# Optimization experiments

Measured on AMD Instinct MI355X. Metric: run time of the kernel, lower is better.

The kernel has to match this reference:

```python
import jax, jax.numpy as jnp
import numpy as np

B, N, C, H = 4, 2048, 1024, 16
D = C // H  # head_dim = 64
SCALE = D ** -0.5


def setup_inputs() -> dict:
    key = jax.random.key(0)
    ks = jax.random.split(key, 7)
    # freqs_cis = exp(i*theta): unit-modulus rotations, as in standard RoPE
    theta = jax.random.uniform(ks[1], (B, N, D // 2), jnp.float32, 0.0, 2 * np.pi)
    return {
        "x": jax.random.normal(ks[0], (B, N, C), jnp.float32),
        "freqs_cos": jnp.cos(theta),
        "freqs_sin": jnp.sin(theta),
        "attn_mask": jax.random.normal(ks[2], (1, 1, N, N), jnp.float32) * 0.1,
        "Wqkv": jax.random.normal(ks[3], (3 * C, C), jnp.float32) * (C ** -0.5),
        "Wproj": jax.random.normal(ks[4], (C, C), jnp.float32) * (C ** -0.5),
        "bproj": jnp.zeros((C,), jnp.float32),
    }


def _rope(t, cos, sin):
    # t: [B,H,N,D]; cos/sin: [B,1,N,D/2]; complex multiply on interleaved pairs
    tr = t.reshape(*t.shape[:-1], D // 2, 2)
    t0, t1 = tr[..., 0], tr[..., 1]
    out = jnp.stack([t0 * cos - t1 * sin, t0 * sin + t1 * cos], axis=-1)
    return out.reshape(t.shape)


def reference(x, freqs_cos, freqs_sin, attn_mask, Wqkv, Wproj, bproj):
    qkv = x @ Wqkv.T  # [B,N,3C]
    qkv = qkv.reshape(B, N, 3, H, D).transpose(2, 0, 3, 1, 4)  # [3,B,H,N,D]
    q, k, v = qkv[0], qkv[1], qkv[2]
    cos = freqs_cos[:, None]  # [B,1,N,D/2]
    sin = freqs_sin[:, None]
    q = _rope(q, cos, sin)
    k = _rope(k, cos, sin)
    attn = jnp.einsum("bhnd,bhmd->bhnm", q * SCALE, k) + attn_mask
    attn = jax.nn.softmax(attn, axis=-1)
    out = jnp.einsum("bhnm,bhmd->bhnd", attn, v)  # [B,H,N,D]
    out = out.transpose(0, 2, 1, 3).reshape(B, N, C)
    return out @ Wproj.T + bproj
```

## Files before the change

kernel.cpp:

```cpp
#include <hip/hip_runtime.h>
#include <hip/hip_bf16.h>
#include <stdint.h>


typedef __bf16 bf16;
typedef __bf16 bf16x4 __attribute__((ext_vector_type(4)));
typedef __bf16 bf16x8 __attribute__((ext_vector_type(8)));
typedef float  f32x4  __attribute__((ext_vector_type(4)));
typedef float  f32x16 __attribute__((ext_vector_type(16)));
typedef int    int4v  __attribute__((ext_vector_type(4)));

#define MFMA16(a, b, c) __builtin_amdgcn_mfma_f32_16x16x32_bf16((a), (b), (c), 0, 0, 0)
#define MFMA32(a, b, c) __builtin_amdgcn_mfma_f32_32x32x16_bf16((a), (b), (c), 0, 0, 0)

__device__ __forceinline__ bf16x4 cvt4s(float a, float b, float c, float d) {
  bf16x4 r;
  r[0] = (bf16)a; r[1] = (bf16)b; r[2] = (bf16)c; r[3] = (bf16)d;
  return r;
}
__device__ __forceinline__ bf16x8 cvt8(f32x4 a, f32x4 b) {
  bf16x8 r;
  r[0] = (bf16)a[0]; r[1] = (bf16)a[1]; r[2] = (bf16)a[2]; r[3] = (bf16)a[3];
  r[4] = (bf16)b[0]; r[5] = (bf16)b[1]; r[6] = (bf16)b[2]; r[7] = (bf16)b[3];
  return r;
}
__device__ __forceinline__ void gload16(const void* g, void* l) {
  __builtin_amdgcn_global_load_lds((const __attribute__((address_space(1))) void*)g,
                                   (__attribute__((address_space(3))) void*)l, 16, 0, 0);
}

__global__ __launch_bounds__(256)
void cvt_k(const float* __restrict__ W, bf16* __restrict__ Wb, float scale)
{
  const size_t i = ((size_t)blockIdx.x * 256 + threadIdx.x) * 8;
  const float* p = W + i;
  f32x4 a = *(const f32x4*)p * scale;
  f32x4 b = *(const f32x4*)(p + 4) * scale;
  *(bf16x8*)(Wb + i) = cvt8(a, b);
}

template<int MODE>
__global__ __launch_bounds__(256)
void gemm_bt(const bf16* __restrict__ A, const bf16* __restrict__ B,
             void* __restrict__ O0, bf16* __restrict__ O1, bf16* __restrict__ O2,
             const float* __restrict__ bias)
{
  constexpr int K = 1024;
  __shared__ __attribute__((aligned(16))) bf16 As[128 * 64];
  __shared__ __attribute__((aligned(16))) bf16 Bs[128 * 64];
  const int tid = threadIdx.x, lane = tid & 63, wid = tid >> 6;
  const int m0 = blockIdx.x * 128, n0 = blockIdx.y * 128;
  const int wm = (wid >> 1) * 64, wn = (wid & 1) * 64;
  const int l15 = lane & 15, lg = lane >> 4;

  f32x4 acc[4][4] = {};

  for (int k0 = 0; k0 < K; k0 += 64) {
#pragma unroll
    for (int c = 0; c < 4; ++c) {
      const int seg = wid * 4 + c;
      const int o = seg * 1024 + lane * 16;
      const int row = o >> 7, colb = o & 127;
      gload16((const char*)B + (((size_t)(n0 + row) * K + k0) << 1) + colb,
              (char*)Bs + seg * 1024);
      gload16((const char*)A + (((size_t)(m0 + row) * K + k0) << 1) + colb,
              (char*)As + seg * 1024);
    }
    __syncthreads();

    bf16x8 af[4][2], bb[4][2];
#pragma unroll
    for (int i = 0; i < 4; ++i)
#pragma unroll
      for (int kk = 0; kk < 2; ++kk) {
        af[i][kk] = *(const bf16x8*)(As + (wm + i * 16 + l15) * 64 + kk * 32 + lg * 8);
        bb[i][kk] = *(const bf16x8*)(Bs + (wn + i * 16 + l15) * 64 + kk * 32 + lg * 8);
      }
#pragma unroll
    for (int mi = 0; mi < 4; ++mi)
#pragma unroll
      for (int ni = 0; ni < 4; ++ni)
#pragma unroll
        for (int kk = 0; kk < 2; ++kk)
          acc[mi][ni] = MFMA16(af[mi][kk], bb[ni][kk], acc[mi][ni]);
    __syncthreads();
  }

#pragma unroll
  for (int mi = 0; mi < 4; ++mi)
#pragma unroll
    for (int ni = 0; ni < 4; ++ni)
#pragma unroll
      for (int r = 0; r < 4; ++r) {
        const int row = m0 + wm + mi * 16 + lg * 4 + r;
        const int col = n0 + wn + ni * 16 + l15;
        float v = acc[mi][ni][r];
        if (MODE == 0) {
          const int s = col >> 10, h = (col >> 6) & 15, d = col & 63;
          const int b = row >> 11, n = row & 2047;
          const bf16 bv = (bf16)v;
          if (s == 0)
            ((bf16*)O0)[(((size_t)(b * 16 + h) * 2048) + n) * 64 + d] = bv;
          else if (s == 1)
            O1[(((size_t)(b * 16 + h) * 2048) + n) * 64 + d] = bv;
          else
            O2[(((size_t)(b * 16 + h) * 64) + d) * 2048 + n] = bv;
        } else {
          ((float*)O0)[(size_t)row * 1024 + col] = v + bias[col];
        }
      }
}

__global__ __launch_bounds__(256)
void rope_k(bf16* __restrict__ Q, bf16* __restrict__ K,
            const float* __restrict__ C, const float* __restrict__ S)
{
  constexpr float SL = 0.125f * 1.4426950408889634f;
  const int gid = blockIdx.x * 256 + threadIdx.x;
  const int part = gid & 3;
  const int rowid = gid >> 2;
  const int n = rowid & 2047;
  const int b = rowid >> 15;
  const size_t cbase = ((size_t)(b * 2048 + n)) * 32 + part * 8;

  float cf[8], sf[8];
  *(f32x4*)cf = *(const f32x4*)(C + cbase);
  *(f32x4*)(cf + 4) = *(const f32x4*)(C + cbase + 4);
  *(f32x4*)sf = *(const f32x4*)(S + cbase);
  *(f32x4*)(sf + 4) = *(const f32x4*)(S + cbase + 4);

  bf16* qp = Q + (size_t)rowid * 64 + part * 16;
  bf16* kp = K + (size_t)rowid * 64 + part * 16;
  __attribute__((aligned(16))) bf16 buf[16];

  *(int4v*)buf = *(const int4v*)qp;
  *(int4v*)(buf + 8) = *(const int4v*)(qp + 8);
#pragma unroll
  for (int j = 0; j < 8; ++j) {
    const float t0 = (float)buf[2 * j], t1 = (float)buf[2 * j + 1];
    buf[2 * j]     = (bf16)((t0 * cf[j] - t1 * sf[j]) * SL);
    buf[2 * j + 1] = (bf16)((t0 * sf[j] + t1 * cf[j]) * SL);
  }
  *(int4v*)qp = *(int4v*)buf;
  *(int4v*)(qp + 8) = *(int4v*)(buf + 8);

  *(int4v*)buf = *(const int4v*)kp;
  *(int4v*)(buf + 8) = *(const int4v*)(kp + 8);
#pragma unroll
  for (int j = 0; j < 8; ++j) {
    const float t0 = (float)buf[2 * j], t1 = (float)buf[2 * j + 1];
    buf[2 * j]     = (bf16)(t0 * cf[j] - t1 * sf[j]);
    buf[2 * j + 1] = (bf16)(t0 * sf[j] + t1 * cf[j]);
  }
  *(int4v*)kp = *(int4v*)buf;
  *(int4v*)(kp + 8) = *(int4v*)(buf + 8);
}

template<int MM>
__global__ __launch_bounds__(256, 4)
void attn_k(const bf16* __restrict__ Q, const bf16* __restrict__ K,
            const bf16* __restrict__ VT, const void* __restrict__ Mv,
            bf16* __restrict__ O)
{
  constexpr float LOG2E = 1.4426950408889634f;
  __shared__ __attribute__((aligned(16))) bf16 SH[9216];
  bf16* Kt = SH;
  bf16* Vt = SH + 4096;

  const int tid = threadIdx.x, lane = tid & 63, w = tid >> 6;
  const int bh = blockIdx.x;
  const int q0 = blockIdx.y * 128;
  const int b = bh >> 4, h = bh & 15;
  const int l31 = lane & 31, hi = lane >> 5;
  const int swz = (l31 & 7) << 3;

  const bf16* Qb = Q + (size_t)bh * 2048 * 64;
  const bf16* Kb = K + (size_t)bh * 2048 * 64;
  const bf16* Vb = VT + (size_t)bh * 64 * 2048;
  const float* Mqf = (const float*)Mv + (size_t)(q0 + w * 32 + l31) * 2048;
  const bf16*  Mqb = (const bf16*)Mv  + (size_t)(q0 + w * 32 + l31) * 2048;

  bf16x8 qf[4];
  {
    const bf16* qr = Qb + (size_t)(q0 + w * 32 + l31) * 64 + 8 * hi;
#pragma unroll
    for (int j = 0; j < 4; ++j) qf[j] = *(const bf16x8*)(qr + 16 * j);
  }

  f32x16 o[2] = {{0,0,0,0,0,0,0,0,0,0,0,0,0,0,0,0},
                 {0,0,0,0,0,0,0,0,0,0,0,0,0,0,0,0}};
  float li = 0.f;

  for (int kv0 = 0; kv0 < 2048; kv0 += 64) {
#pragma unroll
    for (int it = 0; it < 2; ++it) {
      const int idx = it * 256 + tid;
      const int row = idx >> 3, g8 = (idx & 7) * 8;
      const int sc = g8 ^ ((row & 7) << 3);
      *(int4v*)(Kt + row * 64 + sc) =
          *(const int4v*)(Kb + (size_t)(kv0 + row) * 64 + g8);
      *(int4v*)(Vt + row * 64 + sc) =
          *(const int4v*)(Vb + (size_t)row * 2048 + kv0 + g8);
    }

    f32x4 mkf[2][4];
    bf16x4 mkb[2][4];
#pragma unroll
    for (int sub = 0; sub < 2; ++sub)
#pragma unroll
      for (int rg = 0; rg < 4; ++rg) {
        if (MM == 0)
          mkf[sub][rg] = *(const f32x4*)(Mqf + kv0 + 32 * sub + 8 * rg + 4 * hi);
        else
          mkb[sub][rg] = *(const bf16x4*)(Mqb + kv0 + 32 * sub + 8 * rg + 4 * hi);
      }

    __syncthreads();

#pragma unroll
    for (int sub = 0; sub < 2; ++sub) {
      f32x16 s;
#pragma unroll
      for (int rg = 0; rg < 4; ++rg)
#pragma unroll
        for (int i = 0; i < 4; ++i)
          s[4 * rg + i] = (MM == 0) ? mkf[sub][rg][i] * LOG2E
                                    : (float)mkb[sub][rg][i];
      __builtin_amdgcn_s_setprio(1);
#pragma unroll
      for (int j = 0; j < 4; ++j) {
        const bf16x8 kf = *(const bf16x8*)(
            Kt + (sub * 32 + l31) * 64 + ((16 * j + 8 * hi) ^ swz));
        s = MFMA32(kf, qf[j], s);
      }
      __builtin_amdgcn_s_setprio(0);

      float rs = 0.f;
#pragma unroll
      for (int e = 0; e < 16; ++e) {
        const float p = __builtin_exp2f(s[e]);
        s[e] = p;
        rs += p;
      }
      rs += __shfl_xor(rs, 32);
      li += rs;

      uint32_t pk0, pk1, pk2, pk3, pk4, pk5, pk6, pk7;
      asm("v_cvt_pk_bf16_f32 %0, %1, %2" : "=v"(pk0) : "v"(s[0]),  "v"(s[1]));
      asm("v_cvt_pk_bf16_f32 %0, %1, %2" : "=v"(pk1) : "v"(s[2]),  "v"(s[3]));
      asm("v_cvt_pk_bf16_f32 %0, %1, %2" : "=v"(pk2) : "v"(s[4]),  "v"(s[5]));
      asm("v_cvt_pk_bf16_f32 %0, %1, %2" : "=v"(pk3) : "v"(s[6]),  "v"(s[7]));
      asm("v_cvt_pk_bf16_f32 %0, %1, %2" : "=v"(pk4) : "v"(s[8]),  "v"(s[9]));
      asm("v_cvt_pk_bf16_f32 %0, %1, %2" : "=v"(pk5) : "v"(s[10]), "v"(s[11]));
      asm("v_cvt_pk_bf16_f32 %0, %1, %2" : "=v"(pk6) : "v"(s[12]), "v"(s[13]));
      asm("v_cvt_pk_bf16_f32 %0, %1, %2" : "=v"(pk7) : "v"(s[14]), "v"(s[15]));
      asm("v_permlane32_swap_b32 %0, %1" : "+v"(pk0), "+v"(pk2));
      asm("v_permlane32_swap_b32 %0, %1" : "+v"(pk1), "+v"(pk3));
      asm("v_permlane32_swap_b32 %0, %1" : "+v"(pk4), "+v"(pk6));
      asm("v_permlane32_swap_b32 %0, %1" : "+v"(pk5), "+v"(pk7));
      uint32_t pau[2][4] = {{pk0, pk1, pk2, pk3}, {pk4, pk5, pk6, pk7}};
      bf16x8 pa[2];
      __builtin_memcpy(&pa[0], pau[0], 16);
      __builtin_memcpy(&pa[1], pau[1], 16);

      __builtin_amdgcn_s_setprio(1);
#pragma unroll
      for (int kh = 0; kh < 2; ++kh)
#pragma unroll
        for (int dblk = 0; dblk < 2; ++dblk) {
          const bf16x8 vf = *(const bf16x8*)(
              Vt + (dblk * 32 + l31) * 64 + ((sub * 32 + kh * 16 + 8 * hi) ^ swz));
          o[dblk] = MFMA32(vf, pa[kh], o[dblk]);
        }
      __builtin_amdgcn_s_setprio(0);
    }
    __syncthreads();
  }

  const float inv = 1.f / li;
  bf16* ow = SH + w * 2304;
#pragma unroll
  for (int dblk = 0; dblk < 2; ++dblk)
#pragma unroll
    for (int rg = 0; rg < 4; ++rg)
      *(bf16x4*)(ow + l31 * 72 + dblk * 32 + 8 * rg + 4 * hi) =
          cvt4s(o[dblk][4 * rg] * inv, o[dblk][4 * rg + 1] * inv,
                o[dblk][4 * rg + 2] * inv, o[dblk][4 * rg + 3] * inv);
  asm volatile("s_waitcnt lgkmcnt(0)" ::: "memory");
  __builtin_amdgcn_sched_barrier(0);
#pragma unroll
  for (int p = 0; p < 4; ++p) {
    const int row = p * 8 + (lane >> 3);
    const int n = q0 + w * 32 + row;
    const int4v v = *(const int4v*)(ow + row * 72 + (lane & 7) * 8);
    *(int4v*)(O + ((size_t)b * 2048 + n) * 1024 + h * 64 + (lane & 7) * 8) = v;
  }
}

extern "C" void kernel_launch(void* const* d_in, const int* in_sizes, int n_in,
                              void* d_out, int out_size, void* d_ws, size_t ws_size,
                              hipStream_t stream)
{
  (void)in_sizes; (void)n_in; (void)out_size;
  const float* x     = (const float*)d_in[0];
  const float* fcos  = (const float*)d_in[1];
  const float* fsin  = (const float*)d_in[2];
  const float* mask  = (const float*)d_in[3];
  const float* wqkv  = (const float*)d_in[4];
  const float* wproj = (const float*)d_in[5];
  const float* bproj = (const float*)d_in[6];
  float* out = (float*)d_out;

  const size_t SZ  = (size_t)64 * 2048 * 64 * 2;
  const size_t WQB = (size_t)3072 * 1024 * 2;
  const size_t WPB = (size_t)1024 * 1024 * 2;
  const size_t MKB = (size_t)2048 * 2048 * 2;
  const size_t BASE = 4 * SZ + WQB + WPB;
  if (ws_size < BASE) return;
  char* ws = (char*)d_ws;
  bf16* Qr  = (bf16*)(ws);
  bf16* Kr  = (bf16*)(ws + SZ);
  bf16* VT  = (bf16*)(ws + 2 * SZ);
  bf16* Ob  = (bf16*)(ws + 3 * SZ);
  bf16* Wqb = (bf16*)(ws + 4 * SZ);
  bf16* Wpb = (bf16*)(ws + 4 * SZ + WQB);
  bf16* Mb  = (bf16*)(ws + BASE);
  const bool useMb = (ws_size >= BASE + MKB);
  constexpr float LOG2E = 1.4426950408889634f;
  bf16* Xb = Ob;

  cvt_k<<<4096, 256, 0, stream>>>(x, Xb, 1.0f);
  cvt_k<<<1536, 256, 0, stream>>>(wqkv, Wqb, 1.0f);
  cvt_k<<<512, 256, 0, stream>>>(wproj, Wpb, 1.0f);
  if (useMb) cvt_k<<<2048, 256, 0, stream>>>(mask, Mb, LOG2E);
  gemm_bt<0><<<dim3(64, 24), 256, 0, stream>>>(Xb, Wqb, Qr, Kr, VT, nullptr);
  rope_k<<<2048, 256, 0, stream>>>(Qr, Kr, fcos, fsin);
  if (useMb)
    attn_k<1><<<dim3(64, 16), 256, 0, stream>>>(Qr, Kr, VT, Mb, Ob);
  else
    attn_k<0><<<dim3(64, 16), 256, 0, stream>>>(Qr, Kr, VT, mask, Ob);
  gemm_bt<1><<<dim3(64, 8), 256, 0, stream>>>(Ob, Wpb, out, nullptr, nullptr, bproj);
}
```

Baseline: 301.3 us.

## Double-buffer K/V tiles in LDS and prefetch next tile and mask into registers

The attention kernel now prefetches the next K/V tile and attention-mask values into registers while computing on the current tile, then writes them into a second LDS buffer before the barrier. This removes one barrier per iteration and hides global load latency behind the MFMA and softmax work. In exchange it uses more LDS (32KB instead of 18KB) and more registers for the prefetch, which may lower occupancy under launch_bounds(256,4).

```diff
diff --git a/kernel.cpp b/kernel.cpp
--- a/kernel.cpp
+++ b/kernel.cpp
@@ -163,9 +163,8 @@
             bf16* __restrict__ O)
 {
   constexpr float LOG2E = 1.4426950408889634f;
-  __shared__ __attribute__((aligned(16))) bf16 SH[9216];
-  bf16* Kt = SH;
-  bf16* Vt = SH + 4096;
+  constexpr int NT = 32;
+  __shared__ __attribute__((aligned(16))) bf16 SH[16384];
 
   const int tid = threadIdx.x, lane = tid & 63, w = tid >> 6;
   const int bh = blockIdx.x;
@@ -180,42 +179,71 @@
   const float* Mqf = (const float*)Mv + (size_t)(q0 + w * 32 + l31) * 2048;
   const bf16*  Mqb = (const bf16*)Mv  + (size_t)(q0 + w * 32 + l31) * 2048;
 
+  const int srow0 = tid >> 3,          sg8 = (tid & 7) * 8;
+  const int srow1 = (256 + tid) >> 3;
+  const int ssc = sg8 ^ 0;
+
   bf16x8 qf[4];
   {
     const bf16* qr = Qb + (size_t)(q0 + w * 32 + l31) * 64 + 8 * hi;
 #pragma unroll
     for (int j = 0; j < 4; ++j) qf[j] = *(const bf16x8*)(qr + 16 * j);
   }
+  (void)ssc;
 
   f32x16 o[2] = {{0,0,0,0,0,0,0,0,0,0,0,0,0,0,0,0},
                  {0,0,0,0,0,0,0,0,0,0,0,0,0,0,0,0}};
   float li = 0.f;
 
-  for (int kv0 = 0; kv0 < 2048; kv0 += 64) {
-#pragma unroll
-    for (int it = 0; it < 2; ++it) {
-      const int idx = it * 256 + tid;
-      const int row = idx >> 3, g8 = (idx & 7) * 8;
-      const int sc = g8 ^ ((row & 7) << 3);
-      *(int4v*)(Kt + row * 64 + sc) =
-          *(const int4v*)(Kb + (size_t)(kv0 + row) * 64 + g8);
-      *(int4v*)(Vt + row * 64 + sc) =
-          *(const int4v*)(Vb + (size_t)row * 2048 + kv0 + g8);
-    }
-
-    f32x4 mkf[2][4];
-    bf16x4 mkb[2][4];
-#pragma unroll
-    for (int sub = 0; sub < 2; ++sub)
-#pragma unroll
-      for (int rg = 0; rg < 4; ++rg) {
-        if (MM == 0)
-          mkf[sub][rg] = *(const f32x4*)(Mqf + kv0 + 32 * sub + 8 * rg + 4 * hi);
-        else
-          mkb[sub][rg] = *(const bf16x4*)(Mqb + kv0 + 32 * sub + 8 * rg + 4 * hi);
-      }
-
-    __syncthreads();
+  int4v kreg[2], vreg[2];
+  kreg[0] = *(const int4v*)(Kb + (size_t)srow0 * 64 + sg8);
+  kreg[1] = *(const int4v*)(Kb + (size_t)srow1 * 64 + sg8);
+  vreg[0] = *(const int4v*)(Vb + (size_t)srow0 * 2048 + sg8);
+  vreg[1] = *(const int4v*)(Vb + (size_t)srow1 * 2048 + sg8);
+
+  f32x4  mkf_cur[2][4], mkf_nxt[2][4];
+  bf16x4 mkb_cur[2][4], mkb_nxt[2][4];
+#pragma unroll
+  for (int sub = 0; sub < 2; ++sub)
+#pragma unroll
+    for (int rg = 0; rg < 4; ++rg) {
+      if (MM == 0)
+        mkf_cur[sub][rg] = *(const f32x4*)(Mqf + 32 * sub + 8 * rg + 4 * hi);
+      else
+        mkb_cur[sub][rg] = *(const bf16x4*)(Mqb + 32 * sub + 8 * rg + 4 * hi);
+    }
+
+  {
+    bf16* Kt = SH;
+    bf16* Vt = SH + 4096;
+    *(int4v*)(Kt + srow0 * 64 + (sg8 ^ ((srow0 & 7) << 3))) = kreg[0];
+    *(int4v*)(Kt + srow1 * 64 + (sg8 ^ ((srow1 & 7) << 3))) = kreg[1];
+    *(int4v*)(Vt + srow0 * 64 + (sg8 ^ ((srow0 & 7) << 3))) = vreg[0];
+    *(int4v*)(Vt + srow1 * 64 + (sg8 ^ ((srow1 & 7) << 3))) = vreg[1];
+  }
+  __syncthreads();
+
+  for (int t = 0; t < NT; ++t) {
+    const int kv0 = t * 64;
+    bf16* Kt = SH + (t & 1) * 8192;
+    bf16* Vt = Kt + 4096;
+
+    if (t + 1 < NT) {
+      const int kvn = kv0 + 64;
+      kreg[0] = *(const int4v*)(Kb + (size_t)(kvn + srow0) * 64 + sg8);
+      kreg[1] = *(const int4v*)(Kb + (size_t)(kvn + srow1) * 64 + sg8);
+      vreg[0] = *(const int4v*)(Vb + (size_t)srow0 * 2048 + kvn + sg8);
+      vreg[1] = *(const int4v*)(Vb + (size_t)srow1 * 2048 + kvn + sg8);
+#pragma unroll
+      for (int sub = 0; sub < 2; ++sub)
+#pragma unroll
+        for (int rg = 0; rg < 4; ++rg) {
+          if (MM == 0)
+            mkf_nxt[sub][rg] = *(const f32x4*)(Mqf + kvn + 32 * sub + 8 * rg + 4 * hi);
+          else
+            mkb_nxt[sub][rg] = *(const bf16x4*)(Mqb + kvn + 32 * sub + 8 * rg + 4 * hi);
+        }
+    }
 
 #pragma unroll
     for (int sub = 0; sub < 2; ++sub) {
@@ -224,8 +252,8 @@
       for (int rg = 0; rg < 4; ++rg)
 #pragma unroll
         for (int i = 0; i < 4; ++i)
-          s[4 * rg + i] = (MM == 0) ? mkf[sub][rg][i] * LOG2E
-                                    : (float)mkb[sub][rg][i];
+          s[4 * rg + i] = (MM == 0) ? mkf_cur[sub][rg][i] * LOG2E
+                                    : (float)mkb_cur[sub][rg][i];
       __builtin_amdgcn_s_setprio(1);
 #pragma unroll
       for (int j = 0; j < 4; ++j) {
@@ -274,6 +302,22 @@
         }
       __builtin_amdgcn_s_setprio(0);
     }
+
+    if (t + 1 < NT) {
+      bf16* Ktn = SH + ((t + 1) & 1) * 8192;
+      bf16* Vtn = Ktn + 4096;
+      *(int4v*)(Ktn + srow0 * 64 + (sg8 ^ ((srow0 & 7) << 3))) = kreg[0];
+      *(int4v*)(Ktn + srow1 * 64 + (sg8 ^ ((srow1 & 7) << 3))) = kreg[1];
+      *(int4v*)(Vtn + srow0 * 64 + (sg8 ^ ((srow0 & 7) << 3))) = vreg[0];
+      *(int4v*)(Vtn + srow1 * 64 + (sg8 ^ ((srow1 & 7) << 3))) = vreg[1];
+#pragma unroll
+      for (int sub = 0; sub < 2; ++sub)
+#pragma unroll
+        for (int rg = 0; rg < 4; ++rg) {
+          if (MM == 0) mkf_cur[sub][rg] = mkf_nxt[sub][rg];
+          else         mkb_cur[sub][rg] = mkb_nxt[sub][rg];
+        }
+    }
     __syncthreads();
   }
 
```

After: 335.8 us. +11.5%, slower.

## Double-buffer K/V tiles with direct global-to-LDS loads and pre-swizzled layouts

Applied to the files above, without the earlier changes.

Moves the XOR swizzle of K and V^T into the QKV GEMM epilogue and the RoPE kernel, so attention tiles can be copied straight from global memory into LDS with gload16 and no register-side rearrangement. The attention loop becomes a two-stage double buffer: the next K/V tile and the bf16 mask slice are prefetched while the current tile is computed, and one barrier per iteration is dropped. This is meant to hide global load latency behind the MFMA work. In exchange LDS use per block grows to 32 KB, which may lower occupancy, and the K layout now depends on the swizzle staying consistent across three kernels.

```diff
diff --git a/kernel.cpp b/kernel.cpp
--- a/kernel.cpp
+++ b/kernel.cpp
@@ -102,9 +102,10 @@
           if (s == 0)
             ((bf16*)O0)[(((size_t)(b * 16 + h) * 2048) + n) * 64 + d] = bv;
           else if (s == 1)
-            O1[(((size_t)(b * 16 + h) * 2048) + n) * 64 + d] = bv;
+            O1[(((size_t)(b * 16 + h) * 2048) + n) * 64 + (d ^ ((n & 7) << 3))] = bv;
           else
-            O2[(((size_t)(b * 16 + h) * 64) + d) * 2048 + n] = bv;
+            O2[(((size_t)(b * 16 + h) * 64) + d) * 2048 +
+               ((n & ~63) | ((n & 63) ^ ((d & 7) << 3)))] = bv;
         } else {
           ((float*)O0)[(size_t)row * 1024 + col] = v + bias[col];
         }
@@ -121,39 +122,51 @@
   const int rowid = gid >> 2;
   const int n = rowid & 2047;
   const int b = rowid >> 15;
-  const size_t cbase = ((size_t)(b * 2048 + n)) * 32 + part * 8;
-
-  float cf[8], sf[8];
-  *(f32x4*)cf = *(const f32x4*)(C + cbase);
-  *(f32x4*)(cf + 4) = *(const f32x4*)(C + cbase + 4);
-  *(f32x4*)sf = *(const f32x4*)(S + cbase);
-  *(f32x4*)(sf + 4) = *(const f32x4*)(S + cbase + 4);
-
-  bf16* qp = Q + (size_t)rowid * 64 + part * 16;
-  bf16* kp = K + (size_t)rowid * 64 + part * 16;
+  const size_t cb0 = ((size_t)(b * 2048 + n)) * 32;
+
   __attribute__((aligned(16))) bf16 buf[16];
 
-  *(int4v*)buf = *(const int4v*)qp;
-  *(int4v*)(buf + 8) = *(const int4v*)(qp + 8);
-#pragma unroll
-  for (int j = 0; j < 8; ++j) {
-    const float t0 = (float)buf[2 * j], t1 = (float)buf[2 * j + 1];
-    buf[2 * j]     = (bf16)((t0 * cf[j] - t1 * sf[j]) * SL);
-    buf[2 * j + 1] = (bf16)((t0 * sf[j] + t1 * cf[j]) * SL);
-  }
-  *(int4v*)qp = *(int4v*)buf;
-  *(int4v*)(qp + 8) = *(int4v*)(buf + 8);
-
-  *(int4v*)buf = *(const int4v*)kp;
-  *(int4v*)(buf + 8) = *(const int4v*)(kp + 8);
-#pragma unroll
-  for (int j = 0; j < 8; ++j) {
-    const float t0 = (float)buf[2 * j], t1 = (float)buf[2 * j + 1];
-    buf[2 * j]     = (bf16)(t0 * cf[j] - t1 * sf[j]);
-    buf[2 * j + 1] = (bf16)(t0 * sf[j] + t1 * cf[j]);
-  }
-  *(int4v*)kp = *(int4v*)buf;
-  *(int4v*)(kp + 8) = *(int4v*)(buf + 8);
+  {
+    float cf[8], sf[8];
+    *(f32x4*)cf = *(const f32x4*)(C + cb0 + part * 8);
+    *(f32x4*)(cf + 4) = *(const f32x4*)(C + cb0 + part * 8 + 4);
+    *(f32x4*)sf = *(const f32x4*)(S + cb0 + part * 8);
+    *(f32x4*)(sf + 4) = *(const f32x4*)(S + cb0 + part * 8 + 4);
+
+    bf16* qp = Q + (size_t)rowid * 64 + part * 16;
+    *(int4v*)buf = *(const int4v*)qp;
+    *(int4v*)(buf + 8) = *(const int4v*)(qp + 8);
+#pragma unroll
+    for (int j = 0; j < 8; ++j) {
+      const float t0 = (float)buf[2 * j], t1 = (float)buf[2 * j + 1];
+      buf[2 * j]     = (bf16)((t0 * cf[j] - t1 * sf[j]) * SL);
+      buf[2 * j + 1] = (bf16)((t0 * sf[j] + t1 * cf[j]) * SL);
+    }
+    *(int4v*)qp = *(int4v*)buf;
+    *(int4v*)(qp + 8) = *(int4v*)(buf + 8);
+  }
+
+  {
+    const int sg = n & 7;
+    bf16* kp = K + (size_t)rowid * 64 + part * 16;
+    *(int4v*)buf = *(const int4v*)kp;
+    *(int4v*)(buf + 8) = *(const int4v*)(kp + 8);
+#pragma unroll
+    for (int gi = 0; gi < 2; ++gi) {
+      const int lg = (2 * part + gi) ^ sg;
+      const f32x4 c4 = *(const f32x4*)(C + cb0 + lg * 4);
+      const f32x4 s4 = *(const f32x4*)(S + cb0 + lg * 4);
+#pragma unroll
+      for (int m = 0; m < 4; ++m) {
+        const float t0 = (float)buf[gi * 8 + 2 * m];
+        const float t1 = (float)buf[gi * 8 + 2 * m + 1];
+        buf[gi * 8 + 2 * m]     = (bf16)(t0 * c4[m] - t1 * s4[m]);
+        buf[gi * 8 + 2 * m + 1] = (bf16)(t0 * s4[m] + t1 * c4[m]);
+      }
+    }
+    *(int4v*)kp = *(int4v*)buf;
+    *(int4v*)(kp + 8) = *(int4v*)(buf + 8);
+  }
 }
 
 template<int MM>
@@ -163,9 +176,8 @@
             bf16* __restrict__ O)
 {
   constexpr float LOG2E = 1.4426950408889634f;
-  __shared__ __attribute__((aligned(16))) bf16 SH[9216];
-  bf16* Kt = SH;
-  bf16* Vt = SH + 4096;
+  constexpr int NT = 32;
+  __shared__ __attribute__((aligned(16))) bf16 SH[16384];
 
   const int tid = threadIdx.x, lane = tid & 63, w = tid >> 6;
   const int bh = blockIdx.x;
@@ -191,31 +203,56 @@
                  {0,0,0,0,0,0,0,0,0,0,0,0,0,0,0,0}};
   float li = 0.f;
 
-  for (int kv0 = 0; kv0 < 2048; kv0 += 64) {
-#pragma unroll
-    for (int it = 0; it < 2; ++it) {
-      const int idx = it * 256 + tid;
-      const int row = idx >> 3, g8 = (idx & 7) * 8;
-      const int sc = g8 ^ ((row & 7) << 3);
-      *(int4v*)(Kt + row * 64 + sc) =
-          *(const int4v*)(Kb + (size_t)(kv0 + row) * 64 + g8);
-      *(int4v*)(Vt + row * 64 + sc) =
-          *(const int4v*)(Vb + (size_t)row * 2048 + kv0 + g8);
-    }
-
+#define STAGE_TILE(KVN, BUFSEL) do {                                          \
+    bf16* Ktn = SH + (BUFSEL) * 8192;                                         \
+    bf16* Vtn = Ktn + 4096;                                                   \
+    _Pragma("unroll")                                                         \
+    for (int it = 0; it < 2; ++it) {                                          \
+      const int idx = it * 256 + tid;                                         \
+      gload16((const char*)Kb + (((size_t)(KVN) * 64 + idx * 8) << 1),        \
+              (char*)Ktn + it * 4096 + w * 1024);                             \
+      gload16((const char*)Vb +                                               \
+                  (((size_t)(idx >> 3) * 2048 + (KVN) + (idx & 7) * 8) << 1), \
+              (char*)Vtn + it * 4096 + w * 1024);                             \
+    }                                                                         \
+  } while (0)
+
+  bf16x4 mkb_cur[2][4], mkb_nxt[2][4];
+
+  STAGE_TILE(0, 0);
+  if (MM == 1) {
+#pragma unroll
+    for (int sub = 0; sub < 2; ++sub)
+#pragma unroll
+      for (int rg = 0; rg < 4; ++rg)
+        mkb_cur[sub][rg] = *(const bf16x4*)(Mqb + 32 * sub + 8 * rg + 4 * hi);
+  }
+  __syncthreads();
+
+  for (int t = 0; t < NT; ++t) {
+    bf16* Kt = SH + (t & 1) * 8192;
+    bf16* Vt = Kt + 4096;
+
+    if (t + 1 < NT) {
+      const int kvn = (t + 1) * 64;
+      STAGE_TILE(kvn, (t + 1) & 1);
+      if (MM == 1) {
+#pragma unroll
+        for (int sub = 0; sub < 2; ++sub)
+#pragma unroll
+          for (int rg = 0; rg < 4; ++rg)
+            mkb_nxt[sub][rg] = *(const bf16x4*)(Mqb + kvn + 32 * sub + 8 * rg + 4 * hi);
+      }
+    }
     f32x4 mkf[2][4];
-    bf16x4 mkb[2][4];
-#pragma unroll
-    for (int sub = 0; sub < 2; ++sub)
-#pragma unroll
-      for (int rg = 0; rg < 4; ++rg) {
-        if (MM == 0)
+    if (MM == 0) {
+      const int kv0 = t * 64;
+#pragma unroll
+      for (int sub = 0; sub < 2; ++sub)
+#pragma unroll
+        for (int rg = 0; rg < 4; ++rg)
           mkf[sub][rg] = *(const f32x4*)(Mqf + kv0 + 32 * sub + 8 * rg + 4 * hi);
-        else
-          mkb[sub][rg] = *(const bf16x4*)(Mqb + kv0 + 32 * sub + 8 * rg + 4 * hi);
-      }
-
-    __syncthreads();
+    }
 
 #pragma unroll
     for (int sub = 0; sub < 2; ++sub) {
@@ -225,7 +262,7 @@
 #pragma unroll
         for (int i = 0; i < 4; ++i)
           s[4 * rg + i] = (MM == 0) ? mkf[sub][rg][i] * LOG2E
-                                    : (float)mkb[sub][rg][i];
+                                    : (float)mkb_cur[sub][rg][i];
       __builtin_amdgcn_s_setprio(1);
 #pragma unroll
       for (int j = 0; j < 4; ++j) {
@@ -274,8 +311,17 @@
         }
       __builtin_amdgcn_s_setprio(0);
     }
+
+    if (MM == 1 && t + 1 < NT) {
+#pragma unroll
+      for (int sub = 0; sub < 2; ++sub)
+#pragma unroll
+        for (int rg = 0; rg < 4; ++rg)
+          mkb_cur[sub][rg] = mkb_nxt[sub][rg];
+    }
     __syncthreads();
   }
+#undef STAGE_TILE
 
   const float inv = 1.f / li;
   bf16* ow = SH + w * 2304;
```

New measurement: 295.9 us. About the same (-1.8%).
